# Optimization experiments

Hardware: AMD Instinct MI355X
Metric: run time of the kernel (lower is better)

## Reference

```python
import jax, jax.numpy as jnp
import numpy as np

HEADS = 8
EPS = 1e-5


def _attn_axis(x, axis, wq, wkv, wout, bout):
    # x: (B, C, X, Y, Z); self-attention along `axis`, channels at dim 1.
    perm = [0] + [d for d in (2, 3, 4) if d != axis] + [axis, 1]
    xp = jnp.transpose(x, perm)                    # (B, o1, o2, T, C)
    B, o1, o2, T, C = xp.shape
    xf = xp.reshape(B * o1 * o2, T, C)
    q = xf @ wq.T                                  # (Bf, T, C), no bias
    k, v = jnp.split(xf @ wkv.T, 2, axis=-1)
    e = C // HEADS
    sh = lambda t: t.reshape(t.shape[0], T, HEADS, e)
    q, k, v = sh(q), sh(k), sh(v)
    dots = jnp.einsum('bihe,bjhe->bhij', q, k) * (e ** -0.5)
    attn = jax.nn.softmax(dots, axis=-1)
    o = jnp.einsum('bhij,bjhe->bihe', attn, v).reshape(B * o1 * o2, T, C)
    o = (o @ wout.T + bout).reshape(B, o1, o2, T, C)
    inv = tuple(int(i) for i in np.argsort(perm))
    return jnp.transpose(o, inv)


def _ln(x, g, b):
    m = jnp.mean(x, -1, keepdims=True)
    v = jnp.mean((x - m) ** 2, -1, keepdims=True)
    return (x - m) * jax.lax.rsqrt(v + EPS) * g + b


def setup_inputs() -> dict:
    key = jax.random.key(0)
    B, C, X, Y, Z = 2, 128, 48, 48, 48
    ks = iter(jax.random.split(key, 32))
    n = lambda shape, s=0.02: jax.random.normal(next(ks), shape, jnp.float32) * s
    inp = {}
    inp['x'] = jax.random.normal(next(ks), (B, C, X, Y, Z), jnp.float32)
    inp['px'] = jax.random.normal(next(ks), (1, C, X, 1, 1), jnp.float32)
    inp['py'] = jax.random.normal(next(ks), (1, C, 1, Y, 1), jnp.float32)
    inp['pz'] = jax.random.normal(next(ks), (1, C, 1, 1, Z), jnp.float32)
    for i in range(3):
        inp[f'wq{i}'] = n((C, C))
        inp[f'wkv{i}'] = n((2 * C, C))
        inp[f'wout{i}'] = n((C, C))
        inp[f'bout{i}'] = jnp.zeros((C,), jnp.float32)
    inp['ln_g'] = jnp.ones((C,), jnp.float32)
    inp['ln_b'] = jnp.zeros((C,), jnp.float32)
    inp['w1'] = n((C, C)); inp['b1'] = jnp.zeros((C,), jnp.float32)
    inp['w2'] = n((C, C)); inp['b2'] = jnp.zeros((C,), jnp.float32)
    return inp


def reference(x, px, py, pz,
              wq0, wkv0, wout0, bout0,
              wq1, wkv1, wout1, bout1,
              wq2, wkv2, wout2, bout2,
              ln_g, ln_b, w1, b1, w2, b2):
    # source: x += pos_embedding(x); pos_embedding(x) returns x + px + py + pz
    x = x + (x + px + py + pz)
    a = (_attn_axis(x, 2, wq0, wkv0, wout0, bout0)
         + _attn_axis(x, 3, wq1, wkv1, wout1, bout1)
         + _attn_axis(x, 4, wq2, wkv2, wout2, bout2))
    x = a + x                                      # residual (dropout = identity)
    x = jnp.transpose(x, (0, 2, 3, 4, 1))          # channels last
    x = _ln(x, ln_g, ln_b)
    res = x
    h = jax.nn.relu(x @ w1.T + b1)
    h = h @ w2.T + b2
    x = _ln(h + res, ln_g, ln_b)                   # same LayerNorm weights reused
    return jnp.transpose(x, (0, 4, 1, 2, 3))
```

## Files before the change

kernel.cpp:

```cpp
#include <hip/hip_runtime.h>
#include <hip/hip_bf16.h>

typedef __attribute__((ext_vector_type(8))) short short8;
typedef __attribute__((ext_vector_type(4))) short short4v;
typedef __attribute__((ext_vector_type(4))) float floatx4;

#define XSTR 136
#define HSTR 16
#define VSTR 56
#define SSTR 132
#define MSTR 132

static __device__ __forceinline__ short f2b(float f) {
    __hip_bfloat16 h = __float2bfloat16(f);
    return *reinterpret_cast<short*>(&h);
}
static __device__ __forceinline__ float b2f(short s) {
    unsigned int u = ((unsigned int)(unsigned short)s) << 16;
    return __uint_as_float(u);
}

__global__ __launch_bounds__(256) void prep_weights(
    const float* __restrict__ wq0, const float* __restrict__ wkv0,
    const float* __restrict__ wq1, const float* __restrict__ wkv1,
    const float* __restrict__ wq2, const float* __restrict__ wkv2,
    const float* __restrict__ wout0, const float* __restrict__ wout1,
    const float* __restrict__ wout2, const float* __restrict__ w1,
    const float* __restrict__ w2, short* __restrict__ dst)
{
    const int g = blockIdx.x * 256 + threadIdx.x;
    const float* wqs[3]  = { wq0, wq1, wq2 };
    const float* wkvs[3] = { wkv0, wkv1, wkv2 };
    const float* rest[5] = { wout0, wout1, wout2, w1, w2 };
    float val;
    if (g < 147456) {
        const int a = g / 49152, l = g % 49152;
        val = (l < 16384) ? wqs[a][l] : wkvs[a][l - 16384];
    } else {
        const int l = g - 147456;
        val = rest[l >> 14][l & 16383];
    }
    dst[g] = f2b(val);
}

__global__ __launch_bounds__(256) void prep_x2(
    const float* __restrict__ x, const float* __restrict__ px,
    const float* __restrict__ py, const float* __restrict__ pz,
    short* __restrict__ x2b)
{
    __shared__ float tile[128 * 49];
    const int s = blockIdx.x, tid = threadIdx.x;
    const int b = s / 2304, rr = s % 2304, xx = rr / 48, yy = rr % 48;
    for (int f = tid; f < 1536; f += 256) {
        const int c = f / 12, z4 = (f % 12) * 4;
        const floatx4 xv = *(const floatx4*)(x + (long)(b * 128 + c) * 110592 + xx * 2304 + yy * 48 + z4);
        const float pxy = px[c * 48 + xx] + py[c * 48 + yy];
        #pragma unroll
        for (int j = 0; j < 4; ++j)
            tile[c * 49 + z4 + j] = 2.0f * xv[j] + pxy + pz[c * 48 + z4 + j];
    }
    __syncthreads();
    const long tb = (long)b * 110592 + xx * 2304 + yy * 48;
    for (int f = tid; f < 1536; f += 256) {
        const int t = f >> 5, c4 = (f & 31) << 2;
        short4v pk;
        #pragma unroll
        for (int j = 0; j < 4; ++j) pk[j] = f2b(tile[(c4 + j) * 49 + t]);
        *(short4v*)(x2b + (tb + t) * 128 + c4) = pk;
    }
}

template<int AXIS, int ACC>
__global__ __launch_bounds__(512, 4)
void attn_axis(const short* __restrict__ x2b, const short* __restrict__ wcat,
               const short* __restrict__ woutb, const float* __restrict__ bout,
               short* __restrict__ Ab)
{
    __shared__ __align__(16) char SM[79360];
    short* xs  = (short*)SM;
    short* qsT = (short*)(SM + 13056);
    short* ksT = (short*)(SM + 25344);
    short* vs  = (short*)(SM + 37632);
    short* pb  = (short*)(SM + 51968);
    short* obT = (short*)(SM + 66304);
    float* stg = (float*)(SM + 13056);

    const int tid  = threadIdx.x;
    const int lane = tid & 63;
    const int wave = tid >> 6;
    const int l15  = lane & 15;
    const int quad = lane >> 4;

    const int s = blockIdx.x;
    const int b = s / 2304, rr = s % 2304, u = rr / 48, v = rr % 48;
    long base; int stride;
    if (AXIS == 0) { base = (long)b * 110592 + u * 48   + v; stride = 2304; }
    else           { base = (long)b * 110592 + u * 2304 + v; stride = 48;   }

    short4v apre[3];
    if (ACC) {
        #pragma unroll
        for (int i = 0; i < 3; ++i) {
            const int f = tid + i * 512;
            const int t = f >> 5, c4 = (f & 31) << 2;
            apre[i] = *(const short4v*)(Ab + (base + (long)t * stride) * 128 + c4);
        }
    }
    short8 wq_[4], wk_[4], wv_[4];
    {
        const short* wp = wcat + (wave * 16 + l15) * 128 + quad * 8;
        #pragma unroll
        for (int k = 0; k < 4; ++k) wq_[k] = *(const short8*)(wp + k * 32);
    }

    for (int f = tid; f < 1536; f += 512) {
        const int t = f >> 5, c4 = (f & 31) << 2;
        *(short4v*)(xs + t * XSTR + c4) =
            *(const short4v*)(x2b + (base + (long)t * stride) * 128 + c4);
    }
    __syncthreads();

    short8 af[3][4];
    #pragma unroll
    for (int ct = 0; ct < 3; ++ct)
        #pragma unroll
        for (int k = 0; k < 4; ++k)
            af[ct][k] = *(const short8*)(xs + (ct * 16 + l15) * XSTR + k * 32 + quad * 8);

    short* qw  = qsT + wave * (48 * HSTR);
    short* kw  = ksT + wave * (48 * HSTR);
    const int hb = wave * 16;

    {
        const short* wp = wcat + ((wave + 8) * 16 + l15) * 128 + quad * 8;
        #pragma unroll
        for (int k = 0; k < 4; ++k) wk_[k] = *(const short8*)(wp + k * 32);
        floatx4 acc[3] = {{0,0,0,0},{0,0,0,0},{0,0,0,0}};
        #pragma unroll
        for (int ct = 0; ct < 3; ++ct)
            #pragma unroll
            for (int k = 0; k < 4; ++k)
                acc[ct] = __builtin_amdgcn_mfma_f32_16x16x32_bf16(wq_[k], af[ct][k], acc[ct], 0, 0, 0);
        #pragma unroll
        for (int ct = 0; ct < 3; ++ct) {
            short4v pk;
            #pragma unroll
            for (int g = 0; g < 4; ++g) pk[g] = f2b(acc[ct][g] * 0.25f);
            *(short4v*)(qw + (ct * 16 + l15) * HSTR + quad * 4) = pk;
        }
    }
    {
        const short* wp = wcat + ((wave + 16) * 16 + l15) * 128 + quad * 8;
        #pragma unroll
        for (int k = 0; k < 4; ++k) wv_[k] = *(const short8*)(wp + k * 32);
        floatx4 acc[3] = {{0,0,0,0},{0,0,0,0},{0,0,0,0}};
        #pragma unroll
        for (int ct = 0; ct < 3; ++ct)
            #pragma unroll
            for (int k = 0; k < 4; ++k)
                acc[ct] = __builtin_amdgcn_mfma_f32_16x16x32_bf16(wk_[k], af[ct][k], acc[ct], 0, 0, 0);
        #pragma unroll
        for (int ct = 0; ct < 3; ++ct) {
            short4v pk;
            #pragma unroll
            for (int g = 0; g < 4; ++g) pk[g] = f2b(acc[ct][g]);
            *(short4v*)(kw + (ct * 16 + l15) * HSTR + quad * 4) = pk;
        }
    }
    {
        floatx4 acc[3] = {{0,0,0,0},{0,0,0,0},{0,0,0,0}};
        #pragma unroll
        for (int mt = 0; mt < 3; ++mt)
            #pragma unroll
            for (int k = 0; k < 4; ++k)
                acc[mt] = __builtin_amdgcn_mfma_f32_16x16x32_bf16(af[mt][k], wv_[k], acc[mt], 0, 0, 0);
        #pragma unroll
        for (int mt = 0; mt < 3; ++mt) {
            short4v pk;
            #pragma unroll
            for (int g = 0; g < 4; ++g) pk[g] = f2b(acc[mt][g]);
            *(short4v*)(vs + (hb + l15) * VSTR + mt * 16 + quad * 4) = pk;
        }
    }

    short* pbw = pb + wave * (16 * VSTR);
    const short8 Z8 = {0,0,0,0,0,0,0,0};
    short8 akf[3], aqf[3];
    #pragma unroll
    for (int t = 0; t < 3; ++t) {
        akf[t] = (quad < 2) ? *(const short8*)(kw + (t * 16 + l15) * HSTR + quad * 8) : Z8;
        aqf[t] = (quad < 2) ? *(const short8*)(qw + (t * 16 + l15) * HSTR + quad * 8) : Z8;
    }
    short8 av0 = *(const short8*)(vs + (hb + l15) * VSTR + quad * 8);
    short8 av1 = (quad < 2) ? *(const short8*)(vs + (hb + l15) * VSTR + 32 + quad * 8) : Z8;

    #pragma unroll
    for (int it = 0; it < 3; ++it) {
        floatx4 sc[3];
        #pragma unroll
        for (int jt = 0; jt < 3; ++jt) {
            floatx4 z = {0,0,0,0};
            sc[jt] = __builtin_amdgcn_mfma_f32_16x16x32_bf16(akf[jt], aqf[it], z, 0, 0, 0);
        }
        float e[3][4]; float ssum = 0.f;
        #pragma unroll
        for (int jt = 0; jt < 3; ++jt)
            #pragma unroll
            for (int g = 0; g < 4; ++g) { e[jt][g] = __expf(sc[jt][g]); ssum += e[jt][g]; }
        ssum += __shfl_xor(ssum, 16, 64);
        ssum += __shfl_xor(ssum, 32, 64);
        const float inv = 1.0f / ssum;
        #pragma unroll
        for (int jt = 0; jt < 3; ++jt) {
            short4v pk;
            #pragma unroll
            for (int g = 0; g < 4; ++g) pk[g] = f2b(e[jt][g] * inv);
            *(short4v*)(pbw + l15 * VSTR + jt * 16 + quad * 4) = pk;
        }
        short8 ap  = *(const short8*)(pbw + l15 * VSTR + quad * 8);
        short8 ap1 = (quad < 2) ? *(const short8*)(pbw + l15 * VSTR + 32 + quad * 8) : Z8;
        floatx4 o = {0,0,0,0};
        o = __builtin_amdgcn_mfma_f32_16x16x32_bf16(av0, ap,  o, 0, 0, 0);
        o = __builtin_amdgcn_mfma_f32_16x16x32_bf16(av1, ap1, o, 0, 0, 0);
        short4v ok;
        #pragma unroll
        for (int g = 0; g < 4; ++g) ok[g] = f2b(o[g]);
        *(short4v*)(obT + (it * 16 + l15) * XSTR + hb + quad * 4) = ok;
    }
    __syncthreads();

    short8 afo[3][4];
    #pragma unroll
    for (int ct = 0; ct < 3; ++ct)
        #pragma unroll
        for (int k = 0; k < 4; ++k)
            afo[ct][k] = *(const short8*)(obT + (ct * 16 + l15) * XSTR + k * 32 + quad * 8);
    {
        const int nf = wave * 16;
        short8 wo_[4];
        #pragma unroll
        for (int k = 0; k < 4; ++k)
            wo_[k] = *(const short8*)(woutb + (nf + l15) * 128 + k * 32 + quad * 8);
        floatx4 acc[3] = {{0,0,0,0},{0,0,0,0},{0,0,0,0}};
        #pragma unroll
        for (int ct = 0; ct < 3; ++ct)
            #pragma unroll
            for (int k = 0; k < 4; ++k)
                acc[ct] = __builtin_amdgcn_mfma_f32_16x16x32_bf16(wo_[k], afo[ct][k], acc[ct], 0, 0, 0);
        const floatx4 bo4 = *(const floatx4*)(bout + nf + quad * 4);
        #pragma unroll
        for (int ct = 0; ct < 3; ++ct) {
            floatx4 ox;
            #pragma unroll
            for (int g = 0; g < 4; ++g) ox[g] = acc[ct][g] + bo4[g];
            *(floatx4*)(stg + (ct * 16 + l15) * SSTR + nf + quad * 4) = ox;
        }
    }
    __syncthreads();

    #pragma unroll
    for (int i = 0; i < 3; ++i) {
        const int f = tid + i * 512;
        const int t = f >> 5, c4 = (f & 31) << 2;
        const long gi = (base + (long)t * stride) * 128 + c4;
        const floatx4 vv = *(const floatx4*)(stg + t * SSTR + c4);
        short4v out4;
        if (ACC) {
            #pragma unroll
            for (int j = 0; j < 4; ++j) out4[j] = f2b(b2f(apre[i][j]) + vv[j]);
        } else {
            #pragma unroll
            for (int j = 0; j < 4; ++j) out4[j] = f2b(vv[j]);
        }
        *(short4v*)(Ab + gi) = out4;
    }
}

static __device__ __forceinline__ void ln_stats132(const float* xr, float* mean_,
                                                   float* rstd_, int tid)
{
    if (tid < 192) {
        const int r = tid >> 2, p = tid & 3;
        const float* row = xr + r * MSTR + p * 32;
        float s1 = 0.f, s2 = 0.f;
        #pragma unroll
        for (int c0 = 0; c0 < 32; ++c0) {
            const float xv = row[(c0 + p * 8) & 31];
            s1 += xv; s2 += xv * xv;
        }
        s1 += __shfl_xor(s1, 1, 64); s1 += __shfl_xor(s1, 2, 64);
        s2 += __shfl_xor(s2, 1, 64); s2 += __shfl_xor(s2, 2, 64);
        if (p == 0) {
            const float m = s1 * (1.f / 128.f);
            mean_[r] = m;
            rstd_[r] = rsqrtf(s2 * (1.f / 128.f) - m * m + 1e-5f);
        }
    }
}

__global__ __launch_bounds__(512, 4)
void attn2_mlp(const short* __restrict__ x2b, const short* __restrict__ Ab,
               const short* __restrict__ wcat, const short* __restrict__ woutb,
               const float* __restrict__ bout,
               const float* __restrict__ ln_g, const float* __restrict__ ln_b,
               const short* __restrict__ w1b, const float* __restrict__ b1,
               const short* __restrict__ w2b, const float* __restrict__ b2,
               float* __restrict__ out)
{
    __shared__ __align__(16) char SM[81792];
    short* xs   = (short*)SM;
    short* qsT  = (short*)(SM + 13056);
    short* ksT  = (short*)(SM + 25344);
    short* vs   = (short*)(SM + 37632);
    short* pb   = (short*)(SM + 51968);
    short* obT  = (short*)(SM + 66304);
    float* xr   = (float*)(SM + 13056);
    short* lnb  = (short*)(SM + 38400);
    short* hbuf = (short*)(SM + 66304);
    float* gs   = (float*)(SM + 79360);
    float* bs   = (float*)(SM + 79872);
    float* b1s  = (float*)(SM + 80384);
    float* b2s  = (float*)(SM + 80896);
    float* mean_ = (float*)(SM + 81408);
    float* rstd_ = (float*)(SM + 81600);

    const int tid  = threadIdx.x;
    const int lane = tid & 63;
    const int wave = tid >> 6;
    const int l15  = lane & 15;
    const int quad = lane >> 4;

    const int s = blockIdx.x;
    const int b = s / 2304, rr = s % 2304, xx = rr / 48, yy = rr % 48;
    const long tb = (long)b * 110592 + xx * 2304 + yy * 48;

    short4v apre[3];
    #pragma unroll
    for (int i = 0; i < 3; ++i) {
        const int f = tid + i * 512;
        const int t = f >> 5, c4 = (f & 31) << 2;
        apre[i] = *(const short4v*)(Ab + (tb + t) * 128 + c4);
    }
    short8 wq_[4], wk_[4], wv_[4];
    {
        const short* wp = wcat + (wave * 16 + l15) * 128 + quad * 8;
        #pragma unroll
        for (int k = 0; k < 4; ++k) wq_[k] = *(const short8*)(wp + k * 32);
    }

    if (tid < 128) {
        gs[tid] = ln_g[tid]; bs[tid] = ln_b[tid];
        b1s[tid] = b1[tid];  b2s[tid] = b2[tid];
    }
    short4v xpre[3];
    #pragma unroll
    for (int i = 0; i < 3; ++i) {
        const int f = tid + i * 512;
        const int t = f >> 5, c4 = (f & 31) << 2;
        xpre[i] = *(const short4v*)(x2b + (tb + t) * 128 + c4);
        *(short4v*)(xs + t * XSTR + c4) = xpre[i];
    }
    __syncthreads();

    short8 af[3][4];
    #pragma unroll
    for (int ct = 0; ct < 3; ++ct)
        #pragma unroll
        for (int k = 0; k < 4; ++k)
            af[ct][k] = *(const short8*)(xs + (ct * 16 + l15) * XSTR + k * 32 + quad * 8);

    short* qw  = qsT + wave * (48 * HSTR);
    short* kw  = ksT + wave * (48 * HSTR);
    const int hb = wave * 16;

    {
        const short* wp = wcat + ((wave + 8) * 16 + l15) * 128 + quad * 8;
        #pragma unroll
        for (int k = 0; k < 4; ++k) wk_[k] = *(const short8*)(wp + k * 32);
        floatx4 acc[3] = {{0,0,0,0},{0,0,0,0},{0,0,0,0}};
        #pragma unroll
        for (int ct = 0; ct < 3; ++ct)
            #pragma unroll
            for (int k = 0; k < 4; ++k)
                acc[ct] = __builtin_amdgcn_mfma_f32_16x16x32_bf16(wq_[k], af[ct][k], acc[ct], 0, 0, 0);
        #pragma unroll
        for (int ct = 0; ct < 3; ++ct) {
            short4v pk;
            #pragma unroll
            for (int g = 0; g < 4; ++g) pk[g] = f2b(acc[ct][g] * 0.25f);
            *(short4v*)(qw + (ct * 16 + l15) * HSTR + quad * 4) = pk;
        }
    }
    {
        const short* wp = wcat + ((wave + 16) * 16 + l15) * 128 + quad * 8;
        #pragma unroll
        for (int k = 0; k < 4; ++k) wv_[k] = *(const short8*)(wp + k * 32);
        floatx4 acc[3] = {{0,0,0,0},{0,0,0,0},{0,0,0,0}};
        #pragma unroll
        for (int ct = 0; ct < 3; ++ct)
            #pragma unroll
            for (int k = 0; k < 4; ++k)
                acc[ct] = __builtin_amdgcn_mfma_f32_16x16x32_bf16(wk_[k], af[ct][k], acc[ct], 0, 0, 0);
        #pragma unroll
        for (int ct = 0; ct < 3; ++ct) {
            short4v pk;
            #pragma unroll
            for (int g = 0; g < 4; ++g) pk[g] = f2b(acc[ct][g]);
            *(short4v*)(kw + (ct * 16 + l15) * HSTR + quad * 4) = pk;
        }
    }
    {
        floatx4 acc[3] = {{0,0,0,0},{0,0,0,0},{0,0,0,0}};
        #pragma unroll
        for (int mt = 0; mt < 3; ++mt)
            #pragma unroll
            for (int k = 0; k < 4; ++k)
                acc[mt] = __builtin_amdgcn_mfma_f32_16x16x32_bf16(af[mt][k], wv_[k], acc[mt], 0, 0, 0);
        #pragma unroll
        for (int mt = 0; mt < 3; ++mt) {
            short4v pk;
            #pragma unroll
            for (int g = 0; g < 4; ++g) pk[g] = f2b(acc[mt][g]);
            *(short4v*)(vs + (hb + l15) * VSTR + mt * 16 + quad * 4) = pk;
        }
    }

    short* pbw = pb + wave * (16 * VSTR);
    const short8 Z8 = {0,0,0,0,0,0,0,0};
    short8 akf[3], aqf[3];
    #pragma unroll
    for (int t = 0; t < 3; ++t) {
        akf[t] = (quad < 2) ? *(const short8*)(kw + (t * 16 + l15) * HSTR + quad * 8) : Z8;
        aqf[t] = (quad < 2) ? *(const short8*)(qw + (t * 16 + l15) * HSTR + quad * 8) : Z8;
    }
    short8 av0 = *(const short8*)(vs + (hb + l15) * VSTR + quad * 8);
    short8 av1 = (quad < 2) ? *(const short8*)(vs + (hb + l15) * VSTR + 32 + quad * 8) : Z8;

    #pragma unroll
    for (int it = 0; it < 3; ++it) {
        floatx4 sc[3];
        #pragma unroll
        for (int jt = 0; jt < 3; ++jt) {
            floatx4 z = {0,0,0,0};
            sc[jt] = __builtin_amdgcn_mfma_f32_16x16x32_bf16(akf[jt], aqf[it], z, 0, 0, 0);
        }
        float e[3][4]; float ssum = 0.f;
        #pragma unroll
        for (int jt = 0; jt < 3; ++jt)
            #pragma unroll
            for (int g = 0; g < 4; ++g) { e[jt][g] = __expf(sc[jt][g]); ssum += e[jt][g]; }
        ssum += __shfl_xor(ssum, 16, 64);
        ssum += __shfl_xor(ssum, 32, 64);
        const float inv = 1.0f / ssum;
        #pragma unroll
        for (int jt = 0; jt < 3; ++jt) {
            short4v pk;
            #pragma unroll
            for (int g = 0; g < 4; ++g) pk[g] = f2b(e[jt][g] * inv);
            *(short4v*)(pbw + l15 * VSTR + jt * 16 + quad * 4) = pk;
        }
        short8 ap  = *(const short8*)(pbw + l15 * VSTR + quad * 8);
        short8 ap1 = (quad < 2) ? *(const short8*)(pbw + l15 * VSTR + 32 + quad * 8) : Z8;
        floatx4 o = {0,0,0,0};
        o = __builtin_amdgcn_mfma_f32_16x16x32_bf16(av0, ap,  o, 0, 0, 0);
        o = __builtin_amdgcn_mfma_f32_16x16x32_bf16(av1, ap1, o, 0, 0, 0);
        short4v ok;
        #pragma unroll
        for (int g = 0; g < 4; ++g) ok[g] = f2b(o[g]);
        *(short4v*)(obT + (it * 16 + l15) * XSTR + hb + quad * 4) = ok;
    }
    __syncthreads();

    const int nf = wave * 16;
    {
        short8 afo[3][4];
        #pragma unroll
        for (int ct = 0; ct < 3; ++ct)
            #pragma unroll
            for (int k = 0; k < 4; ++k)
                afo[ct][k] = *(const short8*)(obT + (ct * 16 + l15) * XSTR + k * 32 + quad * 8);
        short8 wo_[4];
        #pragma unroll
        for (int k = 0; k < 4; ++k)
            wo_[k] = *(const short8*)(woutb + (nf + l15) * 128 + k * 32 + quad * 8);
        floatx4 acc[3] = {{0,0,0,0},{0,0,0,0},{0,0,0,0}};
        #pragma unroll
        for (int ct = 0; ct < 3; ++ct)
            #pragma unroll
            for (int k = 0; k < 4; ++k)
                acc[ct] = __builtin_amdgcn_mfma_f32_16x16x32_bf16(wo_[k], afo[ct][k], acc[ct], 0, 0, 0);
        const floatx4 bo4 = *(const floatx4*)(bout + nf + quad * 4);
        #pragma unroll
        for (int ct = 0; ct < 3; ++ct) {
            floatx4 ox;
            #pragma unroll
            for (int g = 0; g < 4; ++g) ox[g] = acc[ct][g] + bo4[g];
            *(floatx4*)(xr + (ct * 16 + l15) * MSTR + nf + quad * 4) = ox;
        }
    }
    __syncthreads();

    #pragma unroll
    for (int i = 0; i < 3; ++i) {
        const int f = tid + i * 512;
        const int t = f >> 5, c4 = (f & 31) << 2;
        floatx4 xv = *(const floatx4*)(xr + t * MSTR + c4);
        float s1 = 0.f, s2 = 0.f;
        #pragma unroll
        for (int j = 0; j < 4; ++j) {
            xv[j] += b2f(apre[i][j]) + b2f(xpre[i][j]);
            s1 += xv[j]; s2 += xv[j] * xv[j];
        }
        *(floatx4*)(xr + t * MSTR + c4) = xv;
        s1 += __shfl_xor(s1, 1, 64);  s2 += __shfl_xor(s2, 1, 64);
        s1 += __shfl_xor(s1, 2, 64);  s2 += __shfl_xor(s2, 2, 64);
        s1 += __shfl_xor(s1, 4, 64);  s2 += __shfl_xor(s2, 4, 64);
        s1 += __shfl_xor(s1, 8, 64);  s2 += __shfl_xor(s2, 8, 64);
        s1 += __shfl_xor(s1, 16, 64); s2 += __shfl_xor(s2, 16, 64);
        if ((lane & 31) == 0) {
            const float m = s1 * (1.f / 128.f);
            mean_[t] = m;
            rstd_[t] = rsqrtf(s2 * (1.f / 128.f) - m * m + 1e-5f);
        }
    }
    __syncthreads();

    for (int f = tid; f < 6144; f += 512) {
        const int t = f >> 7, c = f & 127;
        lnb[t * XSTR + c] = f2b((xr[t * MSTR + c] - mean_[t]) * rstd_[t] * gs[c] + bs[c]);
    }
    __syncthreads();

    {
        short8 afl[3][4];
        #pragma unroll
        for (int ct = 0; ct < 3; ++ct)
            #pragma unroll
            for (int k = 0; k < 4; ++k)
                afl[ct][k] = *(const short8*)(lnb + (ct * 16 + l15) * XSTR + k * 32 + quad * 8);
        short8 w1_[4];
        #pragma unroll
        for (int k = 0; k < 4; ++k)
            w1_[k] = *(const short8*)(w1b + (nf + l15) * 128 + k * 32 + quad * 8);
        floatx4 acc[3] = {{0,0,0,0},{0,0,0,0},{0,0,0,0}};
        #pragma unroll
        for (int ct = 0; ct < 3; ++ct)
            #pragma unroll
            for (int k = 0; k < 4; ++k)
                acc[ct] = __builtin_amdgcn_mfma_f32_16x16x32_bf16(w1_[k], afl[ct][k], acc[ct], 0, 0, 0);
        const floatx4 bb4 = *(const floatx4*)(b1s + nf + quad * 4);
        #pragma unroll
        for (int ct = 0; ct < 3; ++ct) {
            short4v hk;
            #pragma unroll
            for (int g = 0; g < 4; ++g) hk[g] = f2b(fmaxf(acc[ct][g] + bb4[g], 0.f));
            *(short4v*)(hbuf + (ct * 16 + l15) * XSTR + nf + quad * 4) = hk;
        }
    }
    __syncthreads();

    {
        short8 afh[3][4];
        #pragma unroll
        for (int ct = 0; ct < 3; ++ct)
            #pragma unroll
            for (int k = 0; k < 4; ++k)
                afh[ct][k] = *(const short8*)(hbuf + (ct * 16 + l15) * XSTR + k * 32 + quad * 8);
        short8 w2_[4];
        #pragma unroll
        for (int k = 0; k < 4; ++k)
            w2_[k] = *(const short8*)(w2b + (nf + l15) * 128 + k * 32 + quad * 8);
        floatx4 acc[3] = {{0,0,0,0},{0,0,0,0},{0,0,0,0}};
        #pragma unroll
        for (int ct = 0; ct < 3; ++ct)
            #pragma unroll
            for (int k = 0; k < 4; ++k)
                acc[ct] = __builtin_amdgcn_mfma_f32_16x16x32_bf16(w2_[k], afh[ct][k], acc[ct], 0, 0, 0);
        const floatx4 bb4 = *(const floatx4*)(b2s + nf + quad * 4);
        const floatx4 g4  = *(const floatx4*)(gs + nf + quad * 4);
        const floatx4 be4 = *(const floatx4*)(bs + nf + quad * 4);
        #pragma unroll
        for (int ct = 0; ct < 3; ++ct) {
            const int t = ct * 16 + l15;
            const float mn = mean_[t], rs = rstd_[t];
            floatx4 xv = *(const floatx4*)(xr + t * MSTR + nf + quad * 4);
            floatx4 nx;
            #pragma unroll
            for (int g = 0; g < 4; ++g) {
                const float ln1 = (xv[g] - mn) * rs * g4[g] + be4[g];
                nx[g] = acc[ct][g] + bb4[g] + ln1;
            }
            *(floatx4*)(xr + t * MSTR + nf + quad * 4) = nx;
        }
    }
    __syncthreads();
    ln_stats132(xr, mean_, rstd_, tid);
    __syncthreads();

    for (int f = tid; f < 1536; f += 512) {
        const int c = f / 12, z4 = (f % 12) * 4;
        floatx4 o4;
        #pragma unroll
        for (int j = 0; j < 4; ++j)
            o4[j] = (xr[(z4 + j) * MSTR + c] - mean_[z4 + j]) * rstd_[z4 + j] * gs[c] + bs[c];
        *(floatx4*)(out + (long)(b * 128 + c) * 110592 + xx * 2304 + yy * 48 + z4) = o4;
    }
}

extern "C" void kernel_launch(void* const* d_in, const int* in_sizes, int n_in,
                              void* d_out, int out_size, void* d_ws, size_t ws_size,
                              hipStream_t stream)
{
    const float* x    = (const float*)d_in[0];
    const float* px   = (const float*)d_in[1];
    const float* py   = (const float*)d_in[2];
    const float* pz   = (const float*)d_in[3];
    const float* wq[3]   = { (const float*)d_in[4],  (const float*)d_in[8],  (const float*)d_in[12] };
    const float* wkv[3]  = { (const float*)d_in[5],  (const float*)d_in[9],  (const float*)d_in[13] };
    const float* wout[3] = { (const float*)d_in[6],  (const float*)d_in[10], (const float*)d_in[14] };
    const float* bout[3] = { (const float*)d_in[7],  (const float*)d_in[11], (const float*)d_in[15] };
    const float* ln_g = (const float*)d_in[16];
    const float* ln_b = (const float*)d_in[17];
    const float* w1   = (const float*)d_in[18];
    const float* b1   = (const float*)d_in[19];
    const float* w2   = (const float*)d_in[20];
    const float* b2   = (const float*)d_in[21];

    short* Ab  = (short*)d_ws;
    short* wb  = (short*)((char*)d_ws + 56623104);
    short* x2b = (short*)((char*)d_ws + 57081856);

    prep_weights<<<896, 256, 0, stream>>>(wq[0], wkv[0], wq[1], wkv[1], wq[2], wkv[2],
                                          wout[0], wout[1], wout[2], w1, w2, wb);
    prep_x2<<<4608, 256, 0, stream>>>(x, px, py, pz, x2b);

    attn_axis<0, 0><<<4608, 512, 0, stream>>>(x2b, wb,         wb + 147456, bout[0], Ab);
    attn_axis<1, 1><<<4608, 512, 0, stream>>>(x2b, wb + 49152, wb + 163840, bout[1], Ab);

    attn2_mlp<<<4608, 512, 0, stream>>>(x2b, Ab, wb + 98304, wb + 180224, bout[2],
                                        ln_g, ln_b, wb + 196608, b1, wb + 212992, b2,
                                        (float*)d_out);
}
```

Measured before the change: 575.0 us.

## Keep Q/K/V and softmax probabilities in registers via lane shuffles, shrink LDS

Q, K, V and the softmax probabilities are now packed into bf16 pairs and redistributed across lanes with __shfl into MFMA operand layout, instead of going through per-wave shared-memory staging buffers. This removes the qsT/ksT/vs/pb LDS regions, shrinking shared memory from about 79-82KB to about 51-54KB per block, and launch_bounds is raised from 4 to 6. The prefetch of the accumulated attention output is moved after the attention phase, and the residual x is re-read from LDS instead of being held in registers. In exchange there are many cross-lane shuffles, and the register budget is tighter under the higher launch bound, which risks spills.

```diff
diff --git a/kernel.cpp b/kernel.cpp
--- a/kernel.cpp
+++ b/kernel.cpp
@@ -4,10 +4,9 @@
 typedef __attribute__((ext_vector_type(8))) short short8;
 typedef __attribute__((ext_vector_type(4))) short short4v;
 typedef __attribute__((ext_vector_type(4))) float floatx4;
+typedef __attribute__((ext_vector_type(4))) int int4v;
 
 #define XSTR 136
-#define HSTR 16
-#define VSTR 56
 #define SSTR 132
 #define MSTR 132
 
@@ -18,6 +17,14 @@
 static __device__ __forceinline__ float b2f(short s) {
     unsigned int u = ((unsigned int)(unsigned short)s) << 16;
     return __uint_as_float(u);
+}
+static __device__ __forceinline__ int pk2(float lo, float hi) {
+    return (int)((((unsigned)(unsigned short)f2b(hi)) << 16) |
+                 (unsigned)(unsigned short)f2b(lo));
+}
+static __device__ __forceinline__ short8 mk8(int a, int b, int c, int d) {
+    int4v t; t[0] = a; t[1] = b; t[2] = c; t[3] = d;
+    return *reinterpret_cast<short8*>(&t);
 }
 
 __global__ __launch_bounds__(256) void prep_weights(
@@ -71,19 +78,15 @@
 }
 
 template<int AXIS, int ACC>
-__global__ __launch_bounds__(512, 4)
+__global__ __launch_bounds__(512, 6)
 void attn_axis(const short* __restrict__ x2b, const short* __restrict__ wcat,
                const short* __restrict__ woutb, const float* __restrict__ bout,
                short* __restrict__ Ab)
 {
-    __shared__ __align__(16) char SM[79360];
+    __shared__ __align__(16) char SM[51456];
     short* xs  = (short*)SM;
-    short* qsT = (short*)(SM + 13056);
-    short* ksT = (short*)(SM + 25344);
-    short* vs  = (short*)(SM + 37632);
-    short* pb  = (short*)(SM + 51968);
-    short* obT = (short*)(SM + 66304);
-    float* stg = (float*)(SM + 13056);
+    short* obT = (short*)(SM + 13056);
+    float* stg = (float*)(SM + 26112);
 
     const int tid  = threadIdx.x;
     const int lane = tid & 63;
@@ -97,6 +100,139 @@
     if (AXIS == 0) { base = (long)b * 110592 + u * 48   + v; stride = 2304; }
     else           { base = (long)b * 110592 + u * 2304 + v; stride = 48;   }
 
+    short8 wq_[4], wk_[4], wv_[4];
+    {
+        const short* wp = wcat + (wave * 16 + l15) * 128 + quad * 8;
+        #pragma unroll
+        for (int k = 0; k < 4; ++k) wq_[k] = *(const short8*)(wp + k * 32);
+    }
+
+    for (int f = tid; f < 1536; f += 512) {
+        const int t = f >> 5, c4 = (f & 31) << 2;
+        *(short4v*)(xs + t * XSTR + c4) =
+            *(const short4v*)(x2b + (base + (long)t * stride) * 128 + c4);
+    }
+    __syncthreads();
+
+    short8 af[3][4];
+    #pragma unroll
+    for (int ct = 0; ct < 3; ++ct)
+        #pragma unroll
+        for (int k = 0; k < 4; ++k)
+            af[ct][k] = *(const short8*)(xs + (ct * 16 + l15) * XSTR + k * 32 + quad * 8);
+
+    int qpk[3][2], kpk[3][2], vpk[3][2];
+    {
+        const short* wp = wcat + ((wave + 8) * 16 + l15) * 128 + quad * 8;
+        #pragma unroll
+        for (int k = 0; k < 4; ++k) wk_[k] = *(const short8*)(wp + k * 32);
+        floatx4 acc[3] = {{0,0,0,0},{0,0,0,0},{0,0,0,0}};
+        #pragma unroll
+        for (int ct = 0; ct < 3; ++ct)
+            #pragma unroll
+            for (int k = 0; k < 4; ++k)
+                acc[ct] = __builtin_amdgcn_mfma_f32_16x16x32_bf16(wq_[k], af[ct][k], acc[ct], 0, 0, 0);
+        #pragma unroll
+        for (int ct = 0; ct < 3; ++ct) {
+            qpk[ct][0] = pk2(acc[ct][0] * 0.25f, acc[ct][1] * 0.25f);
+            qpk[ct][1] = pk2(acc[ct][2] * 0.25f, acc[ct][3] * 0.25f);
+        }
+    }
+    {
+        const short* wp = wcat + ((wave + 16) * 16 + l15) * 128 + quad * 8;
+        #pragma unroll
+        for (int k = 0; k < 4; ++k) wv_[k] = *(const short8*)(wp + k * 32);
+        floatx4 acc[3] = {{0,0,0,0},{0,0,0,0},{0,0,0,0}};
+        #pragma unroll
+        for (int ct = 0; ct < 3; ++ct)
+            #pragma unroll
+            for (int k = 0; k < 4; ++k)
+                acc[ct] = __builtin_amdgcn_mfma_f32_16x16x32_bf16(wk_[k], af[ct][k], acc[ct], 0, 0, 0);
+        #pragma unroll
+        for (int ct = 0; ct < 3; ++ct) {
+            kpk[ct][0] = pk2(acc[ct][0], acc[ct][1]);
+            kpk[ct][1] = pk2(acc[ct][2], acc[ct][3]);
+        }
+    }
+    {
+        floatx4 acc[3] = {{0,0,0,0},{0,0,0,0},{0,0,0,0}};
+        #pragma unroll
+        for (int mt = 0; mt < 3; ++mt)
+            #pragma unroll
+            for (int k = 0; k < 4; ++k)
+                acc[mt] = __builtin_amdgcn_mfma_f32_16x16x32_bf16(af[mt][k], wv_[k], acc[mt], 0, 0, 0);
+        #pragma unroll
+        for (int mt = 0; mt < 3; ++mt) {
+            vpk[mt][0] = pk2(acc[mt][0], acc[mt][1]);
+            vpk[mt][1] = pk2(acc[mt][2], acc[mt][3]);
+        }
+    }
+
+    const short8 Z8 = {0,0,0,0,0,0,0,0};
+    const int qm = quad & 1;
+    const int s0 = l15 + 32 * qm, s1 = s0 + 16;
+    const bool hiq = quad >= 2;
+    short8 aqf[3], akf[3];
+    #pragma unroll
+    for (int t = 0; t < 3; ++t) {
+        short8 q8 = mk8(__shfl(qpk[t][0], s0, 64), __shfl(qpk[t][1], s0, 64),
+                        __shfl(qpk[t][0], s1, 64), __shfl(qpk[t][1], s1, 64));
+        aqf[t] = hiq ? Z8 : q8;
+        akf[t] = mk8(__shfl(kpk[t][0], s0, 64), __shfl(kpk[t][1], s0, 64),
+                     __shfl(kpk[t][0], s1, 64), __shfl(kpk[t][1], s1, 64));
+    }
+    short8 av0, av1;
+    {
+        const int t00 = __shfl(vpk[0][0], s0, 64), t01 = __shfl(vpk[0][1], s0, 64);
+        const int t02 = __shfl(vpk[0][0], s1, 64), t03 = __shfl(vpk[0][1], s1, 64);
+        const int t10 = __shfl(vpk[1][0], s0, 64), t11 = __shfl(vpk[1][1], s0, 64);
+        const int t12 = __shfl(vpk[1][0], s1, 64), t13 = __shfl(vpk[1][1], s1, 64);
+        av0 = mk8(hiq ? t10 : t00, hiq ? t11 : t01, hiq ? t12 : t02, hiq ? t13 : t03);
+        av1 = mk8(__shfl(vpk[2][0], s0, 64), __shfl(vpk[2][1], s0, 64),
+                  __shfl(vpk[2][0], s1, 64), __shfl(vpk[2][1], s1, 64));
+    }
+
+    const int hb = wave * 16;
+    #pragma unroll
+    for (int it = 0; it < 3; ++it) {
+        floatx4 sc[3];
+        #pragma unroll
+        for (int jt = 0; jt < 3; ++jt) {
+            floatx4 z = {0,0,0,0};
+            sc[jt] = __builtin_amdgcn_mfma_f32_16x16x32_bf16(akf[jt], aqf[it], z, 0, 0, 0);
+        }
+        float e[3][4]; float ssum = 0.f;
+        #pragma unroll
+        for (int jt = 0; jt < 3; ++jt)
+            #pragma unroll
+            for (int g = 0; g < 4; ++g) { e[jt][g] = __expf(sc[jt][g]); ssum += e[jt][g]; }
+        ssum += __shfl_xor(ssum, 16, 64);
+        ssum += __shfl_xor(ssum, 32, 64);
+        const float inv = 1.0f / ssum;
+        int ppk[3][2];
+        #pragma unroll
+        for (int jt = 0; jt < 3; ++jt) {
+            ppk[jt][0] = pk2(e[jt][0] * inv, e[jt][1] * inv);
+            ppk[jt][1] = pk2(e[jt][2] * inv, e[jt][3] * inv);
+        }
+        const int a0 = __shfl(ppk[0][0], s0, 64), a1 = __shfl(ppk[0][1], s0, 64);
+        const int a2 = __shfl(ppk[0][0], s1, 64), a3 = __shfl(ppk[0][1], s1, 64);
+        const int c0 = __shfl(ppk[1][0], s0, 64), c1 = __shfl(ppk[1][1], s0, 64);
+        const int c2 = __shfl(ppk[1][0], s1, 64), c3 = __shfl(ppk[1][1], s1, 64);
+        short8 ap  = mk8(hiq ? c0 : a0, hiq ? c1 : a1, hiq ? c2 : a2, hiq ? c3 : a3);
+        short8 ap1 = mk8(__shfl(ppk[2][0], s0, 64), __shfl(ppk[2][1], s0, 64),
+                         __shfl(ppk[2][0], s1, 64), __shfl(ppk[2][1], s1, 64));
+        if (hiq) ap1 = Z8;
+        floatx4 o = {0,0,0,0};
+        o = __builtin_amdgcn_mfma_f32_16x16x32_bf16(av0, ap,  o, 0, 0, 0);
+        o = __builtin_amdgcn_mfma_f32_16x16x32_bf16(av1, ap1, o, 0, 0, 0);
+        short4v ok;
+        #pragma unroll
+        for (int g = 0; g < 4; ++g) ok[g] = f2b(o[g]);
+        *(short4v*)(obT + (it * 16 + l15) * XSTR + hb + quad * 4) = ok;
+    }
+    __syncthreads();
+
     short4v apre[3];
     if (ACC) {
         #pragma unroll
@@ -106,136 +242,14 @@
             apre[i] = *(const short4v*)(Ab + (base + (long)t * stride) * 128 + c4);
         }
     }
-    short8 wq_[4], wk_[4], wv_[4];
-    {
-        const short* wp = wcat + (wave * 16 + l15) * 128 + quad * 8;
-        #pragma unroll
-        for (int k = 0; k < 4; ++k) wq_[k] = *(const short8*)(wp + k * 32);
-    }
-
-    for (int f = tid; f < 1536; f += 512) {
-        const int t = f >> 5, c4 = (f & 31) << 2;
-        *(short4v*)(xs + t * XSTR + c4) =
-            *(const short4v*)(x2b + (base + (long)t * stride) * 128 + c4);
-    }
-    __syncthreads();
-
-    short8 af[3][4];
-    #pragma unroll
-    for (int ct = 0; ct < 3; ++ct)
-        #pragma unroll
-        for (int k = 0; k < 4; ++k)
-            af[ct][k] = *(const short8*)(xs + (ct * 16 + l15) * XSTR + k * 32 + quad * 8);
-
-    short* qw  = qsT + wave * (48 * HSTR);
-    short* kw  = ksT + wave * (48 * HSTR);
-    const int hb = wave * 16;
-
-    {
-        const short* wp = wcat + ((wave + 8) * 16 + l15) * 128 + quad * 8;
-        #pragma unroll
-        for (int k = 0; k < 4; ++k) wk_[k] = *(const short8*)(wp + k * 32);
-        floatx4 acc[3] = {{0,0,0,0},{0,0,0,0},{0,0,0,0}};
-        #pragma unroll
-        for (int ct = 0; ct < 3; ++ct)
-            #pragma unroll
-            for (int k = 0; k < 4; ++k)
-                acc[ct] = __builtin_amdgcn_mfma_f32_16x16x32_bf16(wq_[k], af[ct][k], acc[ct], 0, 0, 0);
-        #pragma unroll
-        for (int ct = 0; ct < 3; ++ct) {
-            short4v pk;
-            #pragma unroll
-            for (int g = 0; g < 4; ++g) pk[g] = f2b(acc[ct][g] * 0.25f);
-            *(short4v*)(qw + (ct * 16 + l15) * HSTR + quad * 4) = pk;
-        }
-    }
-    {
-        const short* wp = wcat + ((wave + 16) * 16 + l15) * 128 + quad * 8;
-        #pragma unroll
-        for (int k = 0; k < 4; ++k) wv_[k] = *(const short8*)(wp + k * 32);
-        floatx4 acc[3] = {{0,0,0,0},{0,0,0,0},{0,0,0,0}};
-        #pragma unroll
-        for (int ct = 0; ct < 3; ++ct)
-            #pragma unroll
-            for (int k = 0; k < 4; ++k)
-                acc[ct] = __builtin_amdgcn_mfma_f32_16x16x32_bf16(wk_[k], af[ct][k], acc[ct], 0, 0, 0);
-        #pragma unroll
-        for (int ct = 0; ct < 3; ++ct) {
-            short4v pk;
-            #pragma unroll
-            for (int g = 0; g < 4; ++g) pk[g] = f2b(acc[ct][g]);
-            *(short4v*)(kw + (ct * 16 + l15) * HSTR + quad * 4) = pk;
-        }
-    }
-    {
-        floatx4 acc[3] = {{0,0,0,0},{0,0,0,0},{0,0,0,0}};
-        #pragma unroll
-        for (int mt = 0; mt < 3; ++mt)
-            #pragma unroll
-            for (int k = 0; k < 4; ++k)
-                acc[mt] = __builtin_amdgcn_mfma_f32_16x16x32_bf16(af[mt][k], wv_[k], acc[mt], 0, 0, 0);
-        #pragma unroll
-        for (int mt = 0; mt < 3; ++mt) {
-            short4v pk;
-            #pragma unroll
-            for (int g = 0; g < 4; ++g) pk[g] = f2b(acc[mt][g]);
-            *(short4v*)(vs + (hb + l15) * VSTR + mt * 16 + quad * 4) = pk;
-        }
-    }
-
-    short* pbw = pb + wave * (16 * VSTR);
-    const short8 Z8 = {0,0,0,0,0,0,0,0};
-    short8 akf[3], aqf[3];
-    #pragma unroll
-    for (int t = 0; t < 3; ++t) {
-        akf[t] = (quad < 2) ? *(const short8*)(kw + (t * 16 + l15) * HSTR + quad * 8) : Z8;
-        aqf[t] = (quad < 2) ? *(const short8*)(qw + (t * 16 + l15) * HSTR + quad * 8) : Z8;
-    }
-    short8 av0 = *(const short8*)(vs + (hb + l15) * VSTR + quad * 8);
-    short8 av1 = (quad < 2) ? *(const short8*)(vs + (hb + l15) * VSTR + 32 + quad * 8) : Z8;
-
-    #pragma unroll
-    for (int it = 0; it < 3; ++it) {
-        floatx4 sc[3];
-        #pragma unroll
-        for (int jt = 0; jt < 3; ++jt) {
-            floatx4 z = {0,0,0,0};
-            sc[jt] = __builtin_amdgcn_mfma_f32_16x16x32_bf16(akf[jt], aqf[it], z, 0, 0, 0);
-        }
-        float e[3][4]; float ssum = 0.f;
-        #pragma unroll
-        for (int jt = 0; jt < 3; ++jt)
-            #pragma unroll
-            for (int g = 0; g < 4; ++g) { e[jt][g] = __expf(sc[jt][g]); ssum += e[jt][g]; }
-        ssum += __shfl_xor(ssum, 16, 64);
-        ssum += __shfl_xor(ssum, 32, 64);
-        const float inv = 1.0f / ssum;
-        #pragma unroll
-        for (int jt = 0; jt < 3; ++jt) {
-            short4v pk;
-            #pragma unroll
-            for (int g = 0; g < 4; ++g) pk[g] = f2b(e[jt][g] * inv);
-            *(short4v*)(pbw + l15 * VSTR + jt * 16 + quad * 4) = pk;
-        }
-        short8 ap  = *(const short8*)(pbw + l15 * VSTR + quad * 8);
-        short8 ap1 = (quad < 2) ? *(const short8*)(pbw + l15 * VSTR + 32 + quad * 8) : Z8;
-        floatx4 o = {0,0,0,0};
-        o = __builtin_amdgcn_mfma_f32_16x16x32_bf16(av0, ap,  o, 0, 0, 0);
-        o = __builtin_amdgcn_mfma_f32_16x16x32_bf16(av1, ap1, o, 0, 0, 0);
-        short4v ok;
-        #pragma unroll
-        for (int g = 0; g < 4; ++g) ok[g] = f2b(o[g]);
-        *(short4v*)(obT + (it * 16 + l15) * XSTR + hb + quad * 4) = ok;
-    }
-    __syncthreads();
-
-    short8 afo[3][4];
-    #pragma unroll
-    for (int ct = 0; ct < 3; ++ct)
-        #pragma unroll
-        for (int k = 0; k < 4; ++k)
-            afo[ct][k] = *(const short8*)(obT + (ct * 16 + l15) * XSTR + k * 32 + quad * 8);
-    {
+
+    {
+        short8 afo[3][4];
+        #pragma unroll
+        for (int ct = 0; ct < 3; ++ct)
+            #pragma unroll
+            for (int k = 0; k < 4; ++k)
+                afo[ct][k] = *(const short8*)(obT + (ct * 16 + l15) * XSTR + k * 32 + quad * 8);
         const int nf = wave * 16;
         short8 wo_[4];
         #pragma unroll
@@ -298,7 +312,7 @@
     }
 }
 
-__global__ __launch_bounds__(512, 4)
+__global__ __launch_bounds__(512, 6)
 void attn2_mlp(const short* __restrict__ x2b, const short* __restrict__ Ab,
                const short* __restrict__ wcat, const short* __restrict__ woutb,
                const float* __restrict__ bout,
@@ -307,22 +321,18 @@
                const short* __restrict__ w2b, const float* __restrict__ b2,
                float* __restrict__ out)
 {
-    __shared__ __align__(16) char SM[81792];
+    __shared__ __align__(16) char SM[53888];
     short* xs   = (short*)SM;
-    short* qsT  = (short*)(SM + 13056);
-    short* ksT  = (short*)(SM + 25344);
-    short* vs   = (short*)(SM + 37632);
-    short* pb   = (short*)(SM + 51968);
-    short* obT  = (short*)(SM + 66304);
-    float* xr   = (float*)(SM + 13056);
-    short* lnb  = (short*)(SM + 38400);
-    short* hbuf = (short*)(SM + 66304);
-    float* gs   = (float*)(SM + 79360);
-    float* bs   = (float*)(SM + 79872);
-    float* b1s  = (float*)(SM + 80384);
-    float* b2s  = (float*)(SM + 80896);
-    float* mean_ = (float*)(SM + 81408);
-    float* rstd_ = (float*)(SM + 81600);
+    short* obT  = (short*)(SM + 13056);
+    float* xr   = (float*)(SM + 26112);
+    short* lnb  = (short*)SM;
+    short* hbuf = (short*)(SM + 13056);
+    float* gs   = (float*)(SM + 51456);
+    float* bs   = (float*)(SM + 51968);
+    float* b1s  = (float*)(SM + 52480);
+    float* b2s  = (float*)(SM + 52992);
+    float* mean_ = (float*)(SM + 53504);
+    float* rstd_ = (float*)(SM + 53696);
 
     const int tid  = threadIdx.x;
     const int lane = tid & 63;
@@ -334,6 +344,142 @@
     const int b = s / 2304, rr = s % 2304, xx = rr / 48, yy = rr % 48;
     const long tb = (long)b * 110592 + xx * 2304 + yy * 48;
 
+    short8 wq_[4], wk_[4], wv_[4];
+    {
+        const short* wp = wcat + (wave * 16 + l15) * 128 + quad * 8;
+        #pragma unroll
+        for (int k = 0; k < 4; ++k) wq_[k] = *(const short8*)(wp + k * 32);
+    }
+
+    if (tid < 128) {
+        gs[tid] = ln_g[tid]; bs[tid] = ln_b[tid];
+        b1s[tid] = b1[tid];  b2s[tid] = b2[tid];
+    }
+    for (int f = tid; f < 1536; f += 512) {
+        const int t = f >> 5, c4 = (f & 31) << 2;
+        *(short4v*)(xs + t * XSTR + c4) = *(const short4v*)(x2b + (tb + t) * 128 + c4);
+    }
+    __syncthreads();
+
+    short8 af[3][4];
+    #pragma unroll
+    for (int ct = 0; ct < 3; ++ct)
+        #pragma unroll
+        for (int k = 0; k < 4; ++k)
+            af[ct][k] = *(const short8*)(xs + (ct * 16 + l15) * XSTR + k * 32 + quad * 8);
+
+    int qpk[3][2], kpk[3][2], vpk[3][2];
+    {
+        const short* wp = wcat + ((wave + 8) * 16 + l15) * 128 + quad * 8;
+        #pragma unroll
+        for (int k = 0; k < 4; ++k) wk_[k] = *(const short8*)(wp + k * 32);
+        floatx4 acc[3] = {{0,0,0,0},{0,0,0,0},{0,0,0,0}};
+        #pragma unroll
+        for (int ct = 0; ct < 3; ++ct)
+            #pragma unroll
+            for (int k = 0; k < 4; ++k)
+                acc[ct] = __builtin_amdgcn_mfma_f32_16x16x32_bf16(wq_[k], af[ct][k], acc[ct], 0, 0, 0);
+        #pragma unroll
+        for (int ct = 0; ct < 3; ++ct) {
+            qpk[ct][0] = pk2(acc[ct][0] * 0.25f, acc[ct][1] * 0.25f);
+            qpk[ct][1] = pk2(acc[ct][2] * 0.25f, acc[ct][3] * 0.25f);
+        }
+    }
+    {
+        const short* wp = wcat + ((wave + 16) * 16 + l15) * 128 + quad * 8;
+        #pragma unroll
+        for (int k = 0; k < 4; ++k) wv_[k] = *(const short8*)(wp + k * 32);
+        floatx4 acc[3] = {{0,0,0,0},{0,0,0,0},{0,0,0,0}};
+        #pragma unroll
+        for (int ct = 0; ct < 3; ++ct)
+            #pragma unroll
+            for (int k = 0; k < 4; ++k)
+                acc[ct] = __builtin_amdgcn_mfma_f32_16x16x32_bf16(wk_[k], af[ct][k], acc[ct], 0, 0, 0);
+        #pragma unroll
+        for (int ct = 0; ct < 3; ++ct) {
+            kpk[ct][0] = pk2(acc[ct][0], acc[ct][1]);
+            kpk[ct][1] = pk2(acc[ct][2], acc[ct][3]);
+        }
+    }
+    {
+        floatx4 acc[3] = {{0,0,0,0},{0,0,0,0},{0,0,0,0}};
+        #pragma unroll
+        for (int mt = 0; mt < 3; ++mt)
+            #pragma unroll
+            for (int k = 0; k < 4; ++k)
+                acc[mt] = __builtin_amdgcn_mfma_f32_16x16x32_bf16(af[mt][k], wv_[k], acc[mt], 0, 0, 0);
+        #pragma unroll
+        for (int mt = 0; mt < 3; ++mt) {
+            vpk[mt][0] = pk2(acc[mt][0], acc[mt][1]);
+            vpk[mt][1] = pk2(acc[mt][2], acc[mt][3]);
+        }
+    }
+
+    const short8 Z8 = {0,0,0,0,0,0,0,0};
+    const int qm = quad & 1;
+    const int s0 = l15 + 32 * qm, s1 = s0 + 16;
+    const bool hiq = quad >= 2;
+    short8 aqf[3], akf[3];
+    #pragma unroll
+    for (int t = 0; t < 3; ++t) {
+        short8 q8 = mk8(__shfl(qpk[t][0], s0, 64), __shfl(qpk[t][1], s0, 64),
+                        __shfl(qpk[t][0], s1, 64), __shfl(qpk[t][1], s1, 64));
+        aqf[t] = hiq ? Z8 : q8;
+        akf[t] = mk8(__shfl(kpk[t][0], s0, 64), __shfl(kpk[t][1], s0, 64),
+                     __shfl(kpk[t][0], s1, 64), __shfl(kpk[t][1], s1, 64));
+    }
+    short8 av0, av1;
+    {
+        const int t00 = __shfl(vpk[0][0], s0, 64), t01 = __shfl(vpk[0][1], s0, 64);
+        const int t02 = __shfl(vpk[0][0], s1, 64), t03 = __shfl(vpk[0][1], s1, 64);
+        const int t10 = __shfl(vpk[1][0], s0, 64), t11 = __shfl(vpk[1][1], s0, 64);
+        const int t12 = __shfl(vpk[1][0], s1, 64), t13 = __shfl(vpk[1][1], s1, 64);
+        av0 = mk8(hiq ? t10 : t00, hiq ? t11 : t01, hiq ? t12 : t02, hiq ? t13 : t03);
+        av1 = mk8(__shfl(vpk[2][0], s0, 64), __shfl(vpk[2][1], s0, 64),
+                  __shfl(vpk[2][0], s1, 64), __shfl(vpk[2][1], s1, 64));
+    }
+
+    const int hb = wave * 16;
+    #pragma unroll
+    for (int it = 0; it < 3; ++it) {
+        floatx4 sc[3];
+        #pragma unroll
+        for (int jt = 0; jt < 3; ++jt) {
+            floatx4 z = {0,0,0,0};
+            sc[jt] = __builtin_amdgcn_mfma_f32_16x16x32_bf16(akf[jt], aqf[it], z, 0, 0, 0);
+        }
+        float e[3][4]; float ssum = 0.f;
+        #pragma unroll
+        for (int jt = 0; jt < 3; ++jt)
+            #pragma unroll
+            for (int g = 0; g < 4; ++g) { e[jt][g] = __expf(sc[jt][g]); ssum += e[jt][g]; }
+        ssum += __shfl_xor(ssum, 16, 64);
+        ssum += __shfl_xor(ssum, 32, 64);
+        const float inv = 1.0f / ssum;
+        int ppk[3][2];
+        #pragma unroll
+        for (int jt = 0; jt < 3; ++jt) {
+            ppk[jt][0] = pk2(e[jt][0] * inv, e[jt][1] * inv);
+            ppk[jt][1] = pk2(e[jt][2] * inv, e[jt][3] * inv);
+        }
+        const int a0 = __shfl(ppk[0][0], s0, 64), a1 = __shfl(ppk[0][1], s0, 64);
+        const int a2 = __shfl(ppk[0][0], s1, 64), a3 = __shfl(ppk[0][1], s1, 64);
+        const int c0 = __shfl(ppk[1][0], s0, 64), c1 = __shfl(ppk[1][1], s0, 64);
+        const int c2 = __shfl(ppk[1][0], s1, 64), c3 = __shfl(ppk[1][1], s1, 64);
+        short8 ap  = mk8(hiq ? c0 : a0, hiq ? c1 : a1, hiq ? c2 : a2, hiq ? c3 : a3);
+        short8 ap1 = mk8(__shfl(ppk[2][0], s0, 64), __shfl(ppk[2][1], s0, 64),
+                         __shfl(ppk[2][0], s1, 64), __shfl(ppk[2][1], s1, 64));
+        if (hiq) ap1 = Z8;
+        floatx4 o = {0,0,0,0};
+        o = __builtin_amdgcn_mfma_f32_16x16x32_bf16(av0, ap,  o, 0, 0, 0);
+        o = __builtin_amdgcn_mfma_f32_16x16x32_bf16(av1, ap1, o, 0, 0, 0);
+        short4v ok;
+        #pragma unroll
+        for (int g = 0; g < 4; ++g) ok[g] = f2b(o[g]);
+        *(short4v*)(obT + (it * 16 + l15) * XSTR + hb + quad * 4) = ok;
+    }
+    __syncthreads();
+
     short4v apre[3];
     #pragma unroll
     for (int i = 0; i < 3; ++i) {
@@ -341,135 +487,6 @@
         const int t = f >> 5, c4 = (f & 31) << 2;
         apre[i] = *(const short4v*)(Ab + (tb + t) * 128 + c4);
     }
-    short8 wq_[4], wk_[4], wv_[4];
-    {
-        const short* wp = wcat + (wave * 16 + l15) * 128 + quad * 8;
-        #pragma unroll
-        for (int k = 0; k < 4; ++k) wq_[k] = *(const short8*)(wp + k * 32);
-    }
-
-    if (tid < 128) {
-        gs[tid] = ln_g[tid]; bs[tid] = ln_b[tid];
-        b1s[tid] = b1[tid];  b2s[tid] = b2[tid];
-    }
-    short4v xpre[3];
-    #pragma unroll
-    for (int i = 0; i < 3; ++i) {
-        const int f = tid + i * 512;
-        const int t = f >> 5, c4 = (f & 31) << 2;
-        xpre[i] = *(const short4v*)(x2b + (tb + t) * 128 + c4);
-        *(short4v*)(xs + t * XSTR + c4) = xpre[i];
-    }
-    __syncthreads();
-
-    short8 af[3][4];
-    #pragma unroll
-    for (int ct = 0; ct < 3; ++ct)
-        #pragma unroll
-        for (int k = 0; k < 4; ++k)
-            af[ct][k] = *(const short8*)(xs + (ct * 16 + l15) * XSTR + k * 32 + quad * 8);
-
-    short* qw  = qsT + wave * (48 * HSTR);
-    short* kw  = ksT + wave * (48 * HSTR);
-    const int hb = wave * 16;
-
-    {
-        const short* wp = wcat + ((wave + 8) * 16 + l15) * 128 + quad * 8;
-        #pragma unroll
-        for (int k = 0; k < 4; ++k) wk_[k] = *(const short8*)(wp + k * 32);
-        floatx4 acc[3] = {{0,0,0,0},{0,0,0,0},{0,0,0,0}};
-        #pragma unroll
-        for (int ct = 0; ct < 3; ++ct)
-            #pragma unroll
-            for (int k = 0; k < 4; ++k)
-                acc[ct] = __builtin_amdgcn_mfma_f32_16x16x32_bf16(wq_[k], af[ct][k], acc[ct], 0, 0, 0);
-        #pragma unroll
-        for (int ct = 0; ct < 3; ++ct) {
-            short4v pk;
-            #pragma unroll
-            for (int g = 0; g < 4; ++g) pk[g] = f2b(acc[ct][g] * 0.25f);
-            *(short4v*)(qw + (ct * 16 + l15) * HSTR + quad * 4) = pk;
-        }
-    }
-    {
-        const short* wp = wcat + ((wave + 16) * 16 + l15) * 128 + quad * 8;
-        #pragma unroll
-        for (int k = 0; k < 4; ++k) wv_[k] = *(const short8*)(wp + k * 32);
-        floatx4 acc[3] = {{0,0,0,0},{0,0,0,0},{0,0,0,0}};
-        #pragma unroll
-        for (int ct = 0; ct < 3; ++ct)
-            #pragma unroll
-            for (int k = 0; k < 4; ++k)
-                acc[ct] = __builtin_amdgcn_mfma_f32_16x16x32_bf16(wk_[k], af[ct][k], acc[ct], 0, 0, 0);
-        #pragma unroll
-        for (int ct = 0; ct < 3; ++ct) {
-            short4v pk;
-            #pragma unroll
-            for (int g = 0; g < 4; ++g) pk[g] = f2b(acc[ct][g]);
-            *(short4v*)(kw + (ct * 16 + l15) * HSTR + quad * 4) = pk;
-        }
-    }
-    {
-        floatx4 acc[3] = {{0,0,0,0},{0,0,0,0},{0,0,0,0}};
-        #pragma unroll
-        for (int mt = 0; mt < 3; ++mt)
-            #pragma unroll
-            for (int k = 0; k < 4; ++k)
-                acc[mt] = __builtin_amdgcn_mfma_f32_16x16x32_bf16(af[mt][k], wv_[k], acc[mt], 0, 0, 0);
-        #pragma unroll
-        for (int mt = 0; mt < 3; ++mt) {
-            short4v pk;
-            #pragma unroll
-            for (int g = 0; g < 4; ++g) pk[g] = f2b(acc[mt][g]);
-            *(short4v*)(vs + (hb + l15) * VSTR + mt * 16 + quad * 4) = pk;
-        }
-    }
-
-    short* pbw = pb + wave * (16 * VSTR);
-    const short8 Z8 = {0,0,0,0,0,0,0,0};
-    short8 akf[3], aqf[3];
-    #pragma unroll
-    for (int t = 0; t < 3; ++t) {
-        akf[t] = (quad < 2) ? *(const short8*)(kw + (t * 16 + l15) * HSTR + quad * 8) : Z8;
-        aqf[t] = (quad < 2) ? *(const short8*)(qw + (t * 16 + l15) * HSTR + quad * 8) : Z8;
-    }
-    short8 av0 = *(const short8*)(vs + (hb + l15) * VSTR + quad * 8);
-    short8 av1 = (quad < 2) ? *(const short8*)(vs + (hb + l15) * VSTR + 32 + quad * 8) : Z8;
-
-    #pragma unroll
-    for (int it = 0; it < 3; ++it) {
-        floatx4 sc[3];
-        #pragma unroll
-        for (int jt = 0; jt < 3; ++jt) {
-            floatx4 z = {0,0,0,0};
-            sc[jt] = __builtin_amdgcn_mfma_f32_16x16x32_bf16(akf[jt], aqf[it], z, 0, 0, 0);
-        }
-        float e[3][4]; float ssum = 0.f;
-        #pragma unroll
-        for (int jt = 0; jt < 3; ++jt)
-            #pragma unroll
-            for (int g = 0; g < 4; ++g) { e[jt][g] = __expf(sc[jt][g]); ssum += e[jt][g]; }
-        ssum += __shfl_xor(ssum, 16, 64);
-        ssum += __shfl_xor(ssum, 32, 64);
-        const float inv = 1.0f / ssum;
-        #pragma unroll
-        for (int jt = 0; jt < 3; ++jt) {
-            short4v pk;
-            #pragma unroll
-            for (int g = 0; g < 4; ++g) pk[g] = f2b(e[jt][g] * inv);
-            *(short4v*)(pbw + l15 * VSTR + jt * 16 + quad * 4) = pk;
-        }
-        short8 ap  = *(const short8*)(pbw + l15 * VSTR + quad * 8);
-        short8 ap1 = (quad < 2) ? *(const short8*)(pbw + l15 * VSTR + 32 + quad * 8) : Z8;
-        floatx4 o = {0,0,0,0};
-        o = __builtin_amdgcn_mfma_f32_16x16x32_bf16(av0, ap,  o, 0, 0, 0);
-        o = __builtin_amdgcn_mfma_f32_16x16x32_bf16(av1, ap1, o, 0, 0, 0);
-        short4v ok;
-        #pragma unroll
-        for (int g = 0; g < 4; ++g) ok[g] = f2b(o[g]);
-        *(short4v*)(obT + (it * 16 + l15) * XSTR + hb + quad * 4) = ok;
-    }
-    __syncthreads();
 
     const int nf = wave * 16;
     {
@@ -505,10 +522,11 @@
         const int f = tid + i * 512;
         const int t = f >> 5, c4 = (f & 31) << 2;
         floatx4 xv = *(const floatx4*)(xr + t * MSTR + c4);
+        const short4v x4 = *(const short4v*)(xs + t * XSTR + c4);
         float s1 = 0.f, s2 = 0.f;
         #pragma unroll
         for (int j = 0; j < 4; ++j) {
-            xv[j] += b2f(apre[i][j]) + b2f(xpre[i][j]);
+            xv[j] += b2f(apre[i][j]) + b2f(x4[j]);
             s1 += xv[j]; s2 += xv[j] * xv[j];
         }
         *(floatx4*)(xr + t * MSTR + c4) = xv;
```

New measurement: 628.4 us. +9.3%, slower.
